# Optimization experiments

Hardware: AMD Instinct MI355X
Metric: run time of the kernel (lower is better)

## Reference

```python
import jax, jax.numpy as jnp
import numpy as np

BS, P, D = 64, 300, 1024
NUM_CLASSES = 150


def setup_inputs() -> dict:
    key = jax.random.key(0)
    ks = jax.random.split(key, 12)
    s = 0.02
    return {
        "x": jax.random.normal(ks[0], (BS * P, D), jnp.float32),
        "subject": jax.random.normal(ks[1], (BS, D), jnp.float32),
        "obj": jax.random.normal(ks[2], (BS, D), jnp.float32),
        "relation": jax.random.normal(ks[3], (BS, D), jnp.float32),
        "W_theta": jax.random.normal(ks[4], (D, D), jnp.float32) * s,
        "b_theta": jax.random.normal(ks[5], (D,), jnp.float32) * s,
        "W_pair": jax.random.normal(ks[6], (3 * D, 1), jnp.float32) * s,
        "b_pair": jax.random.normal(ks[7], (1,), jnp.float32) * s,
        "W_cls": jax.random.normal(ks[8], (2 * D, 1), jnp.float32) * s,
        "b_cls": jax.random.normal(ks[9], (1,), jnp.float32) * s,
        "W_bbox": jax.random.normal(ks[10], (D, (NUM_CLASSES + 1) * 4), jnp.float32) * s,
        "b_bbox": jax.random.normal(ks[11], ((NUM_CLASSES + 1) * 4,), jnp.float32) * s,
    }


def reference(x, subject, obj, relation, W_theta, b_theta, W_pair, b_pair,
              W_cls, b_cls, W_bbox, b_bbox):
    bs = relation.shape[0]
    rel = relation @ W_theta + b_theta  # (bs, D)
    xb = x.reshape(bs, P, D)

    # cls_score_pair(concat([x1, x2, rel])) decomposed into 3 sliced matmuls.
    # x1[b,i,j] = x[b,j] (cols), x2[b,i,j] = x[b,i] (rows).
    Wa, Wb, Wc = W_pair[:D, 0], W_pair[D:2 * D, 0], W_pair[2 * D:, 0]
    col_term = xb @ Wa          # (bs, P) -> broadcast over rows i
    row_term = xb @ Wb          # (bs, P) -> broadcast over cols j
    rel_term = rel @ Wc + b_pair[0]  # (bs,)
    pair_score = jax.nn.sigmoid(row_term[:, :, None] + col_term[None if False else slice(None), None, :]
                                + rel_term[:, None, None])  # (bs, P, P)

    # cls_score on [x, subject] and [x, object]
    W1, W2 = W_cls[:D, 0], W_cls[D:, 0]
    xw = xb @ W1                                  # (bs, P)
    s_score = jax.nn.sigmoid(xw + (subject @ W2 + b_cls[0])[:, None])  # (bs, P)
    o_score = jax.nn.sigmoid(xw + (obj @ W2 + b_cls[0])[:, None])      # (bs, P)

    pair_score = pair_score * o_score[:, None, :] * s_score[:, :, None]

    x_subj = jnp.stack([1.0 - s_score, s_score], axis=-1).reshape(-1, 2)
    x_obj = jnp.stack([1.0 - o_score, o_score], axis=-1).reshape(-1, 2)

    bbox_deltas = x @ W_bbox + b_bbox  # (bs*P, (C+1)*4)
    return (x_subj, x_obj, pair_score, bbox_deltas)
```

## Files before the change

kernel.cpp:

```cpp
#include <hip/hip_runtime.h>

#define PP    300
#define DD    1024
#define NOUT  604
#define NROWS 19200
#define OFF_PAIR  76800
#define OFF_BBOX  5836800

typedef unsigned short u16;
typedef __attribute__((ext_vector_type(8))) short bf16x8;
typedef __attribute__((ext_vector_type(4))) float f32x4;

#define GLOBAL_AS __attribute__((address_space(1)))
#define LDS_AS    __attribute__((address_space(3)))

__device__ inline u16 f2bf(float f) {
    unsigned u = __float_as_uint(f);
    return (u16)((u + 0x7fffu + ((u >> 16) & 1u)) >> 16);
}
__device__ inline float dot4(float4 a, float4 b) {
    return fmaf(a.x, b.x, fmaf(a.y, b.y, fmaf(a.z, b.z, a.w * b.w)));
}
__device__ inline float sigmoidf(float z) { return 1.f / (1.f + __expf(-z)); }

__global__ void k_transpose(const float* __restrict__ W, u16* __restrict__ Bt) {
    __shared__ float tile[32][33];
    int k0 = blockIdx.x * 32;
    int n0 = blockIdx.y * 32;
    int tx = threadIdx.x;
    int ty = threadIdx.y;
#pragma unroll
    for (int i = 0; i < 4; ++i) {
        int k = k0 + ty + i * 8;
        int n = n0 + tx;
        tile[ty + i * 8][tx] = (n < NOUT) ? W[(size_t)k * NOUT + n] : 0.f;
    }
    __syncthreads();
#pragma unroll
    for (int i = 0; i < 4; ++i) {
        int n = n0 + ty + i * 8;
        int k = k0 + tx;
        Bt[(size_t)n * DD + k] = f2bf(tile[tx][ty + i * 8]);
    }
}

__global__ void k_vtheta(const float* __restrict__ Wt, const float* __restrict__ Wpair,
                         float* __restrict__ v) {
    int wave = threadIdx.x >> 6, lane = threadIdx.x & 63;
    int k = blockIdx.x * 4 + wave;
    const float4* row = (const float4*)(Wt + (size_t)k * DD);
    const float4* wc  = (const float4*)(Wpair + 2 * DD);
    float s = 0.f;
#pragma unroll
    for (int i = 0; i < 4; ++i) s += dot4(row[i * 64 + lane], wc[i * 64 + lane]);
#pragma unroll
    for (int off = 32; off; off >>= 1) s += __shfl_down(s, off, 64);
    if (lane == 0) v[k] = s;
}

__global__ void k_scalars(const float* __restrict__ relation, const float* __restrict__ subject,
                          const float* __restrict__ obj, const float* __restrict__ btheta,
                          const float* __restrict__ Wpair, const float* __restrict__ bpair,
                          const float* __restrict__ Wcls, const float* __restrict__ bcls,
                          const float* __restrict__ v,
                          float* __restrict__ relt, float* __restrict__ subc,
                          float* __restrict__ objc) {
    __shared__ float red[4];
    int wave = threadIdx.x >> 6, lane = threadIdx.x & 63;
    int b = blockIdx.x;
    const float4* aa;
    const float4* bb;
    if (wave == 0)      { aa = (const float4*)(relation + (size_t)b * DD); bb = (const float4*)v; }
    else if (wave == 1) { aa = (const float4*)(subject + (size_t)b * DD);  bb = (const float4*)(Wcls + DD); }
    else if (wave == 2) { aa = (const float4*)(obj + (size_t)b * DD);      bb = (const float4*)(Wcls + DD); }
    else                { aa = (const float4*)btheta;                      bb = (const float4*)(Wpair + 2 * DD); }
    float s = 0.f;
#pragma unroll
    for (int i = 0; i < 4; ++i) s += dot4(aa[i * 64 + lane], bb[i * 64 + lane]);
#pragma unroll
    for (int off = 32; off; off >>= 1) s += __shfl_down(s, off, 64);
    if (lane == 0) red[wave] = s;
    __syncthreads();
    if (threadIdx.x == 0) {
        relt[b] = red[0] + red[3] + bpair[0];
        subc[b] = red[1] + bcls[0];
        objc[b] = red[2] + bcls[0];
    }
}

__global__ __launch_bounds__(256) void k_rows(
        const float* __restrict__ x, const float* __restrict__ Wpair,
        const float* __restrict__ Wcls,
        const float* __restrict__ relt, const float* __restrict__ subc,
        const float* __restrict__ objc,
        float* __restrict__ colv, float* __restrict__ rowp,
        float* __restrict__ sarr, float* __restrict__ oarr,
        float* __restrict__ out) {
    int wave = threadIdx.x >> 6, lane = threadIdx.x & 63;
    int r = blockIdx.x * 4 + wave;
    const float4* xr = (const float4*)(x + (size_t)r * DD);
    const float4* wa = (const float4*)(Wpair);
    const float4* wb = (const float4*)(Wpair + DD);
    const float4* w1 = (const float4*)(Wcls);
    float ca = 0.f, cb = 0.f, cw = 0.f;
#pragma unroll
    for (int i = 0; i < 4; ++i) {
        int idx = i * 64 + lane;
        float4 xv = xr[idx];
        ca += dot4(xv, wa[idx]);
        cb += dot4(xv, wb[idx]);
        cw += dot4(xv, w1[idx]);
    }
#pragma unroll
    for (int off = 32; off; off >>= 1) {
        ca += __shfl_down(ca, off, 64);
        cb += __shfl_down(cb, off, 64);
        cw += __shfl_down(cw, off, 64);
    }
    if (lane == 0) {
        int b = r / 300;
        float s = sigmoidf(cw + subc[b]);
        float o = sigmoidf(cw + objc[b]);
        colv[r] = ca;
        rowp[r] = cb + relt[b];
        sarr[r] = s;
        oarr[r] = o;
        ((float2*)out)[r]         = make_float2(1.f - s, s);
        ((float2*)out)[NROWS + r] = make_float2(1.f - o, o);
    }
}

__global__ __launch_bounds__(192) void k_pair(
        const float* __restrict__ rowp, const float* __restrict__ colv,
        const float* __restrict__ sarr, const float* __restrict__ oarr,
        float* __restrict__ pout) {
    int r = blockIdx.x;
    int b = r / 300;
    int j = threadIdx.x;
    if (j >= 150) return;
    float rp = rowp[r];
    float ss = sarr[r];
    const float* cb = colv + b * 300;
    const float* ob = oarr + b * 300;
    float p0 = sigmoidf(rp + cb[2 * j])     * ob[2 * j]     * ss;
    float p1 = sigmoidf(rp + cb[2 * j + 1]) * ob[2 * j + 1] * ss;
    ((float2*)(pout + (size_t)r * 300))[j] = make_float2(p0, p1);
}

#define BKK 64
__global__ __launch_bounds__(256) void k_gemm(
        const float* __restrict__ x, const u16* __restrict__ bt,
        const float* __restrict__ bias, float* __restrict__ out) {
    __shared__ u16 As[128 * BKK] __attribute__((aligned(16)));
    __shared__ u16 Bs[128 * BKK] __attribute__((aligned(16)));

    int bid = blockIdx.x;
    int xcd = bid & 7;
    int rest = bid >> 3;
    int n_t = rest % 5;
    int m_t = (rest / 5) * 8 + xcd;
    if (m_t >= 150) return;

    int tid = threadIdx.x;
    int wave = tid >> 6;
    int lane = tid & 63;
    int wr = wave >> 1, wc = wave & 1;
    int quad = lane >> 4;
    int l16 = lane & 15;

    f32x4 acc[4][4] = {};

    const float* a_base = x  + (size_t)m_t * 128 * DD;
    const u16*   b_base = bt + (size_t)n_t * 128 * DD;
    int s_row = lane >> 3;
    int s_c16 = lane & 7;
    int arow8 = tid >> 4;
    int acol4 = tid & 15;

    for (int k0 = 0; k0 < DD; k0 += BKK) {
#pragma unroll
        for (int q = 0; q < 4; ++q) {
            int rowblk = q * 32 + wave * 8;
            const u16* gb = b_base + (size_t)(rowblk + s_row) * DD + k0 + s_c16 * 8;
            __builtin_amdgcn_global_load_lds((const GLOBAL_AS unsigned int*)gb,
                                             (LDS_AS unsigned int*)(Bs + rowblk * BKK),
                                             16, 0, 0);
        }
#pragma unroll
        for (int it = 0; it < 8; ++it) {
            int row = it * 16 + arow8;
            float4 av = *(const float4*)(a_base + (size_t)row * DD + k0 + acol4 * 4);
            unsigned lo = __builtin_amdgcn_perm(__float_as_uint(av.y), __float_as_uint(av.x), 0x07060302u);
            unsigned hi = __builtin_amdgcn_perm(__float_as_uint(av.w), __float_as_uint(av.z), 0x07060302u);
            *(uint2*)(As + row * BKK + acol4 * 4) = make_uint2(lo, hi);
        }
        __syncthreads();
#pragma unroll
        for (int kk = 0; kk < BKK; kk += 32) {
            bf16x8 af[4], bfv[4];
#pragma unroll
            for (int f = 0; f < 4; ++f) {
                int m = wr * 64 + f * 16 + l16;
                af[f] = *(const bf16x8*)(As + m * BKK + kk + quad * 8);
                int n = wc * 64 + f * 16 + l16;
                bfv[f] = *(const bf16x8*)(Bs + n * BKK + kk + quad * 8);
            }
#pragma unroll
            for (int fi = 0; fi < 4; ++fi)
#pragma unroll
                for (int fj = 0; fj < 4; ++fj)
                    acc[fi][fj] = __builtin_amdgcn_mfma_f32_16x16x32_bf16(
                        af[fi], bfv[fj], acc[fi][fj], 0, 0, 0);
        }
        __syncthreads();
    }

#pragma unroll
    for (int fj = 0; fj < 4; ++fj) {
        int col = n_t * 128 + wc * 64 + fj * 16 + l16;
        if (col < NOUT) {
            float bia = bias[col];
#pragma unroll
            for (int fi = 0; fi < 4; ++fi) {
#pragma unroll
                for (int rg = 0; rg < 4; ++rg) {
                    int row = m_t * 128 + wr * 64 + fi * 16 + quad * 4 + rg;
                    out[(size_t)row * NOUT + col] = acc[fi][fj][rg] + bia;
                }
            }
        }
    }
}

extern "C" void kernel_launch(void* const* d_in, const int* in_sizes, int n_in,
                              void* d_out, int out_size, void* d_ws, size_t ws_size,
                              hipStream_t stream) {
    const void* P[12] = {};
    int sv[3] = {-1, -1, -1}; int nsv = 0;
    int sc[2] = {-1, -1};     int nsc = 0;
    for (int i = 0; i < n_in; ++i) {
        switch (in_sizes[i]) {
            case 19660800: P[0]  = d_in[i]; break;
            case 65536:    if (nsv < 3) sv[nsv++] = i; break;
            case 1048576:  P[4]  = d_in[i]; break;
            case 1024:     P[5]  = d_in[i]; break;
            case 3072:     P[6]  = d_in[i]; break;
            case 1:        if (nsc < 2) sc[nsc++] = i; break;
            case 2048:     P[8]  = d_in[i]; break;
            case 618496:   P[10] = d_in[i]; break;
            case 604:      P[11] = d_in[i]; break;
            default: break;
        }
    }
    bool alpha = (n_in == 12 && in_sizes[0] == 618496);
    if (alpha) {
        P[2] = d_in[sv[0]]; P[3] = d_in[sv[1]]; P[1] = d_in[sv[2]];
        P[9] = d_in[sc[0]]; P[7] = d_in[sc[1]];
    } else {
        P[1] = d_in[sv[0]]; P[2] = d_in[sv[1]]; P[3] = d_in[sv[2]];
        P[7] = d_in[sc[0]]; P[9] = d_in[sc[1]];
    }
    const float* x        = (const float*)P[0];
    const float* subject  = (const float*)P[1];
    const float* obj      = (const float*)P[2];
    const float* relation = (const float*)P[3];
    const float* W_theta  = (const float*)P[4];
    const float* b_theta  = (const float*)P[5];
    const float* W_pair   = (const float*)P[6];
    const float* b_pair   = (const float*)P[7];
    const float* W_cls    = (const float*)P[8];
    const float* b_cls    = (const float*)P[9];
    const float* W_bbox   = (const float*)P[10];
    const float* b_bbox   = (const float*)P[11];
    float* out = (float*)d_out;

    char* ws = (char*)d_ws;
    float* v    = (float*)(ws + 0);
    float* relt = (float*)(ws + 4096);
    float* subc = (float*)(ws + 4352);
    float* objc = (float*)(ws + 4608);
    float* colv = (float*)(ws + 4864);
    float* rowp = (float*)(ws + 81664);
    float* sarr = (float*)(ws + 158464);
    float* oarr = (float*)(ws + 235264);
    u16*   Bt   = (u16*)(ws + 312064);

    k_transpose<<<dim3(32, 20), dim3(32, 8), 0, stream>>>(W_bbox, Bt);
    k_vtheta<<<256, 256, 0, stream>>>(W_theta, W_pair, v);
    k_scalars<<<64, 256, 0, stream>>>(relation, subject, obj, b_theta, W_pair, b_pair,
                                      W_cls, b_cls, v, relt, subc, objc);
    k_rows<<<4800, 256, 0, stream>>>(x, W_pair, W_cls, relt, subc, objc,
                                     colv, rowp, sarr, oarr, out);
    k_pair<<<19200, 192, 0, stream>>>(rowp, colv, sarr, oarr, out + OFF_PAIR);
    k_gemm<<<760, 256, 0, stream>>>(x, Bt, b_bbox, out + OFF_BBOX);
}
```

Baseline: 233.9 us.

## Emit bf16 copy of x in row pass and use async-LDS bf16 GEMM; batch pair rows

The row-reduction kernel now also writes a bf16 copy of x while it already has x in registers. A new GEMM reads that copy with global_load_lds straight into LDS, so it no longer converts fp32 to bf16 inside the GEMM and reads half the bytes. The pair kernel now handles 10 rows per block with the column and object vectors staged in shared memory, cutting block count and redundant loads. The bf16 path depends on the workspace being large enough and falls back to the old GEMM otherwise, and it adds the cost of writing and rereading about 40MB of extra traffic.

Measured after the change: 233.2 us. Within noise of the previous version (-0.3%).

```diff
diff --git a/kernel.cpp b/kernel.cpp
--- a/kernel.cpp
+++ b/kernel.cpp
@@ -88,6 +88,7 @@
     }
 }
 
+template<int WB>
 __global__ __launch_bounds__(256) void k_rows(
         const float* __restrict__ x, const float* __restrict__ Wpair,
         const float* __restrict__ Wcls,
@@ -95,7 +96,7 @@
         const float* __restrict__ objc,
         float* __restrict__ colv, float* __restrict__ rowp,
         float* __restrict__ sarr, float* __restrict__ oarr,
-        float* __restrict__ out) {
+        float* __restrict__ out, u16* __restrict__ xb) {
     int wave = threadIdx.x >> 6, lane = threadIdx.x & 63;
     int r = blockIdx.x * 4 + wave;
     const float4* xr = (const float4*)(x + (size_t)r * DD);
@@ -110,6 +111,11 @@
         ca += dot4(xv, wa[idx]);
         cb += dot4(xv, wb[idx]);
         cw += dot4(xv, w1[idx]);
+        if (WB) {
+            unsigned lo = __builtin_amdgcn_perm(__float_as_uint(xv.y), __float_as_uint(xv.x), 0x07060302u);
+            unsigned hi = __builtin_amdgcn_perm(__float_as_uint(xv.w), __float_as_uint(xv.z), 0x07060302u);
+            *(uint2*)(xb + (size_t)r * DD + idx * 4) = make_uint2(lo, hi);
+        }
     }
 #pragma unroll
     for (int off = 32; off; off >>= 1) {
@@ -130,24 +136,117 @@
     }
 }
 
+#define PR_ROWS 10
 __global__ __launch_bounds__(192) void k_pair(
         const float* __restrict__ rowp, const float* __restrict__ colv,
         const float* __restrict__ sarr, const float* __restrict__ oarr,
         float* __restrict__ pout) {
-    int r = blockIdx.x;
-    int b = r / 300;
-    int j = threadIdx.x;
-    if (j >= 150) return;
-    float rp = rowp[r];
-    float ss = sarr[r];
-    const float* cb = colv + b * 300;
-    const float* ob = oarr + b * 300;
-    float p0 = sigmoidf(rp + cb[2 * j])     * ob[2 * j]     * ss;
-    float p1 = sigmoidf(rp + cb[2 * j + 1]) * ob[2 * j + 1] * ss;
-    ((float2*)(pout + (size_t)r * 300))[j] = make_float2(p0, p1);
+    __shared__ float cb_s[300];
+    __shared__ float ob_s[300];
+    int blk = blockIdx.x;
+    int b = blk / 30;
+    int chunk = blk - b * 30;
+    int r0 = b * 300 + chunk * PR_ROWS;
+    int tid = threadIdx.x;
+    for (int j = tid; j < 300; j += 192) {
+        cb_s[j] = colv[b * 300 + j];
+        ob_s[j] = oarr[b * 300 + j];
+    }
+    __syncthreads();
+    if (tid < 150) {
+        float c0 = cb_s[2 * tid],     c1 = cb_s[2 * tid + 1];
+        float o0 = ob_s[2 * tid],     o1 = ob_s[2 * tid + 1];
+#pragma unroll
+        for (int rr = 0; rr < PR_ROWS; ++rr) {
+            int r = r0 + rr;
+            float rp = rowp[r];
+            float ss = sarr[r];
+            float p0 = sigmoidf(rp + c0) * o0 * ss;
+            float p1 = sigmoidf(rp + c1) * o1 * ss;
+            ((float2*)(pout + (size_t)r * 300))[tid] = make_float2(p0, p1);
+        }
+    }
 }
 
 #define BKK 64
+__global__ __launch_bounds__(256) void k_gemm_bf(
+        const u16* __restrict__ xb, const u16* __restrict__ bt,
+        const float* __restrict__ bias, float* __restrict__ out) {
+    __shared__ u16 As[128 * BKK] __attribute__((aligned(16)));
+    __shared__ u16 Bs[128 * BKK] __attribute__((aligned(16)));
+
+    int bid = blockIdx.x;
+    int xcd = bid & 7;
+    int rest = bid >> 3;
+    int n_t = rest % 5;
+    int m_t = (rest / 5) * 8 + xcd;
+    if (m_t >= 150) return;
+
+    int tid = threadIdx.x;
+    int wave = tid >> 6;
+    int lane = tid & 63;
+    int wr = wave >> 1, wc = wave & 1;
+    int quad = lane >> 4;
+    int l16 = lane & 15;
+
+    f32x4 acc[4][4] = {};
+
+    const u16* a_base = xb + (size_t)m_t * 128 * DD;
+    const u16* b_base = bt + (size_t)n_t * 128 * DD;
+    int s_row = lane >> 3;
+    int s_c16 = lane & 7;
+
+    for (int k0 = 0; k0 < DD; k0 += BKK) {
+#pragma unroll
+        for (int q = 0; q < 4; ++q) {
+            int rowblk = q * 32 + wave * 8;
+            const u16* ga = a_base + (size_t)(rowblk + s_row) * DD + k0 + s_c16 * 8;
+            __builtin_amdgcn_global_load_lds((const GLOBAL_AS unsigned int*)ga,
+                                             (LDS_AS unsigned int*)(As + rowblk * BKK),
+                                             16, 0, 0);
+            const u16* gb = b_base + (size_t)(rowblk + s_row) * DD + k0 + s_c16 * 8;
+            __builtin_amdgcn_global_load_lds((const GLOBAL_AS unsigned int*)gb,
+                                             (LDS_AS unsigned int*)(Bs + rowblk * BKK),
+                                             16, 0, 0);
+        }
+        __syncthreads();
+#pragma unroll
+        for (int kk = 0; kk < BKK; kk += 32) {
+            bf16x8 af[4], bfv[4];
+#pragma unroll
+            for (int f = 0; f < 4; ++f) {
+                int m = wr * 64 + f * 16 + l16;
+                af[f] = *(const bf16x8*)(As + m * BKK + kk + quad * 8);
+                int n = wc * 64 + f * 16 + l16;
+                bfv[f] = *(const bf16x8*)(Bs + n * BKK + kk + quad * 8);
+            }
+#pragma unroll
+            for (int fi = 0; fi < 4; ++fi)
+#pragma unroll
+                for (int fj = 0; fj < 4; ++fj)
+                    acc[fi][fj] = __builtin_amdgcn_mfma_f32_16x16x32_bf16(
+                        af[fi], bfv[fj], acc[fi][fj], 0, 0, 0);
+        }
+        __syncthreads();
+    }
+
+#pragma unroll
+    for (int fj = 0; fj < 4; ++fj) {
+        int col = n_t * 128 + wc * 64 + fj * 16 + l16;
+        if (col < NOUT) {
+            float bia = bias[col];
+#pragma unroll
+            for (int fi = 0; fi < 4; ++fi) {
+#pragma unroll
+                for (int rg = 0; rg < 4; ++rg) {
+                    int row = m_t * 128 + wr * 64 + fi * 16 + quad * 4 + rg;
+                    out[(size_t)row * NOUT + col] = acc[fi][fj][rg] + bia;
+                }
+            }
+        }
+    }
+}
+
 __global__ __launch_bounds__(256) void k_gemm(
         const float* __restrict__ x, const u16* __restrict__ bt,
         const float* __restrict__ bias, float* __restrict__ out) {
@@ -284,13 +383,26 @@
     float* sarr = (float*)(ws + 158464);
     float* oarr = (float*)(ws + 235264);
     u16*   Bt   = (u16*)(ws + 312064);
+    u16*   Xb   = (u16*)(ws + 1622784);
+
+    const size_t WS_NEED_BF16 = 40944384;
+    bool big_ws = (ws_size >= WS_NEED_BF16);
 
     k_transpose<<<dim3(32, 20), dim3(32, 8), 0, stream>>>(W_bbox, Bt);
     k_vtheta<<<256, 256, 0, stream>>>(W_theta, W_pair, v);
     k_scalars<<<64, 256, 0, stream>>>(relation, subject, obj, b_theta, W_pair, b_pair,
                                       W_cls, b_cls, v, relt, subc, objc);
-    k_rows<<<4800, 256, 0, stream>>>(x, W_pair, W_cls, relt, subc, objc,
-                                     colv, rowp, sarr, oarr, out);
-    k_pair<<<19200, 192, 0, stream>>>(rowp, colv, sarr, oarr, out + OFF_PAIR);
-    k_gemm<<<760, 256, 0, stream>>>(x, Bt, b_bbox, out + OFF_BBOX);
-}
+    if (big_ws) {
+        k_rows<1><<<4800, 256, 0, stream>>>(x, W_pair, W_cls, relt, subc, objc,
+                                            colv, rowp, sarr, oarr, out, Xb);
+    } else {
+        k_rows<0><<<4800, 256, 0, stream>>>(x, W_pair, W_cls, relt, subc, objc,
+                                            colv, rowp, sarr, oarr, out, nullptr);
+    }
+    k_pair<<<1920, 192, 0, stream>>>(rowp, colv, sarr, oarr, out + OFF_PAIR);
+    if (big_ws) {
+        k_gemm_bf<<<760, 256, 0, stream>>>(Xb, Bt, b_bbox, out + OFF_BBOX);
+    } else {
+        k_gemm<<<760, 256, 0, stream>>>(x, Bt, b_bbox, out + OFF_BBOX);
+    }
+}
```
